# Kernel tuning notes

Measured on AMD Instinct MI355X. Metric: run time of the kernel, lower is better.

The kernel has to match this reference:

```python
import jax, jax.numpy as jnp
import numpy as np

H = 1024


def setup_inputs() -> dict:
    key = jax.random.key(0)
    ks = jax.random.split(key, 7)
    x = jax.random.normal(ks[0], (8, 2048, H), dtype=jnp.float32)
    s = 1.0 / np.sqrt(H)
    Wq = jax.random.normal(ks[1], (H, H), dtype=jnp.float32) * s
    bq = jnp.zeros((H,), dtype=jnp.float32)
    Wk = jax.random.normal(ks[2], (H, H), dtype=jnp.float32) * s
    bk = jnp.zeros((H,), dtype=jnp.float32)
    Wv = jax.random.normal(ks[3], (H, H), dtype=jnp.float32) * s
    bv = jnp.zeros((H,), dtype=jnp.float32)
    return {"x": x, "Wq": Wq, "bq": bq, "Wk": Wk, "bk": bk, "Wv": Wv, "bv": bv}


def reference(x, Wq, bq, Wk, bk, Wv, bv):
    # q,k,v: [B,S,H]
    q = jnp.einsum('bsh,hd->bsd', x, Wq) + bq
    k = jnp.einsum('bsh,hd->bsd', x, Wk) + bk
    v = jnp.einsum('bsh,hd->bsd', x, Wv) + bv
    scale = 1.0 / jnp.sqrt(jnp.asarray(x.shape[-1], dtype=x.dtype))
    scores = jnp.einsum('bqd,bkd->bqk', q, k) * scale  # [B,S,S]
    attn = jax.nn.softmax(scores, axis=-1)
    return jnp.einsum('bqk,bkd->bqd', attn, v)
```

## Files before the change

kernel.cpp:

```cpp
#include <hip/hip_runtime.h>

typedef _Float16 half8  __attribute__((ext_vector_type(8)));
typedef _Float16 half4v __attribute__((ext_vector_type(4)));
typedef float    floatx4 __attribute__((ext_vector_type(4)));

#define GLD_LDS16(g, l)                                                        \
  __builtin_amdgcn_global_load_lds(                                            \
      (const __attribute__((address_space(1))) void*)(g),                      \
      (__attribute__((address_space(3))) void*)(l), 16, 0, 0)

#define SBAR() __builtin_amdgcn_s_barrier()
#define WAITVM2() asm volatile("s_waitcnt vmcnt(2)" ::: "memory")
#define WAITVM0() asm volatile("s_waitcnt vmcnt(0)" ::: "memory")
#define SCHED0() __builtin_amdgcn_sched_barrier(0)


#define STG_A(c, ht, ko)                                                       \
  do {                                                                         \
    GLD_LDS16(A0 + (size_t)(ht) * lda128 + (ko),                               \
              &lds[(c) * 32768 + ((ht) * 1024 + wid * 128) * 8]);              \
    GLD_LDS16(A1 + (size_t)(ht) * lda128 + (ko),                               \
              &lds[(c) * 32768 + ((ht) * 1024 + wid * 128 + 64) * 8]);         \
  } while (0)
#define STG_B(c, ht, ko)                                                       \
  do {                                                                         \
    GLD_LDS16(B0 + (size_t)(ht) * ldb128 + (ko),                               \
              &lds[(c) * 32768 + 16384 + ((ht) * 1024 + wid * 128) * 8]);      \
    GLD_LDS16(B1 + (size_t)(ht) * ldb128 + (ko),                               \
              &lds[(c) * 32768 + 16384 + ((ht) * 1024 + wid * 128 + 64) * 8]); \
  } while (0)

#define RDA(dst, c, mt, ks)                                                    \
  do {                                                                         \
    const int ra_ = wm + (mt) * 16 + lr;                                       \
    dst = *(const half8*)&lds[(c) * 32768 +                                    \
                              (ra_ * 8 + (((ks) * 4 + lk) ^ (ra_ & 7))) * 8];  \
  } while (0)
#define RDB(dst, c, nt, ks)                                                    \
  do {                                                                         \
    const int rb_ = wn + (nt) * 16 + lr;                                       \
    dst = *(const half8*)&lds[(c) * 32768 + 16384 +                            \
                              (rb_ * 8 + (((ks) * 4 + lk) ^ (rb_ & 7))) * 8];  \
  } while (0)

#define MM4x2(MB, NB, BF)                                                      \
  do {                                                                         \
    _Pragma("unroll") for (int mt_ = 0; mt_ < 4; ++mt_)                        \
        _Pragma("unroll") for (int n_ = 0; n_ < 2; ++n_)                       \
            _Pragma("unroll") for (int ks_ = 0; ks_ < 2; ++ks_)                \
                acc[(MB) + mt_][(NB) + n_] =                                   \
        __builtin_amdgcn_mfma_f32_16x16x32_f16(                                \
            af[mt_][ks_], BF[n_][ks_], acc[(MB) + mt_][(NB) + n_], 0, 0, 0);   \
  } while (0)

#define KBLOCK(CUR, KT)                                                        \
  do {                                                                         \
    const int ko_ = ((KT) + 1) << 6;                                           \
    const bool pf_ = ((KT) + 1 < NT);                                          \
       \
    if (pf_) {                                                                 \
      STG_A(1 - (CUR), 0, ko_);                                                \
      WAITVM2();                                                               \
    } else {                                                                   \
      WAITVM0();                                                               \
    }                                                                          \
    SBAR();                                                                    \
    SCHED0();                                                                  \
    RDA(af[0][0], CUR, 0, 0); RDA(af[0][1], CUR, 0, 1);                        \
    RDA(af[1][0], CUR, 1, 0); RDA(af[1][1], CUR, 1, 1);                        \
    RDA(af[2][0], CUR, 2, 0); RDA(af[2][1], CUR, 2, 1);                        \
    RDA(af[3][0], CUR, 3, 0); RDA(af[3][1], CUR, 3, 1);                        \
    RDB(bf0[0][0], CUR, 0, 0); RDB(bf0[0][1], CUR, 0, 1);                      \
    RDB(bf0[1][0], CUR, 1, 0); RDB(bf0[1][1], CUR, 1, 1);                      \
    SBAR();                                                                    \
    SCHED0();                                                                  \
    __builtin_amdgcn_s_setprio(1);                                             \
    MM4x2(0, 0, bf0);                                                          \
    __builtin_amdgcn_s_setprio(0);                                             \
    SBAR();                                                                    \
                \
    RDB(bf1[0][0], CUR, 2, 0); RDB(bf1[0][1], CUR, 2, 1);                      \
    RDB(bf1[1][0], CUR, 3, 0); RDB(bf1[1][1], CUR, 3, 1);                      \
    if (pf_) STG_B(1 - (CUR), 0, ko_);                                         \
    SBAR();                                                                    \
    SCHED0();                                                                  \
    __builtin_amdgcn_s_setprio(1);                                             \
    MM4x2(0, 2, bf1);                                                          \
    __builtin_amdgcn_s_setprio(0);                                             \
    SBAR();                                                                    \
                        \
    RDA(af[0][0], CUR, 4, 0); RDA(af[0][1], CUR, 4, 1);                        \
    RDA(af[1][0], CUR, 5, 0); RDA(af[1][1], CUR, 5, 1);                        \
    RDA(af[2][0], CUR, 6, 0); RDA(af[2][1], CUR, 6, 1);                        \
    RDA(af[3][0], CUR, 7, 0); RDA(af[3][1], CUR, 7, 1);                        \
    if (pf_) STG_A(1 - (CUR), 1, ko_);                                         \
    SBAR();                                                                    \
    SCHED0();                                                                  \
    __builtin_amdgcn_s_setprio(1);                                             \
    MM4x2(4, 2, bf1);                                                          \
    __builtin_amdgcn_s_setprio(0);                                             \
    SBAR();                                                                    \
             \
    if (pf_) STG_B(1 - (CUR), 1, ko_);                                         \
    SBAR();                                                                    \
    SCHED0();                                                                  \
    __builtin_amdgcn_s_setprio(1);                                             \
    MM4x2(4, 0, bf0);                                                          \
    __builtin_amdgcn_s_setprio(0);                                             \
    SBAR();                                                                    \
  } while (0)

template <int EPI>
__global__ __launch_bounds__(512, 2) void gemm_bt(
    const _Float16* __restrict__ A, const _Float16* __restrict__ B,
    void* __restrict__ Cv, void* __restrict__ Cv2, int lda, int ldb, int ldc,
    int kdim, long long sAz, long long sBz, long long sCz,
    const float* __restrict__ b0, const float* __restrict__ b1,
    const float* __restrict__ b2, float* __restrict__ rowsum, float scale) {
  __shared__ _Float16 lds[65536];

  const int bid = blockIdx.x;
  int z, m0, n0;
  if (EPI == 0) {
    const int xcd = bid & 7, j = bid >> 3;
    z = j >> 5;
    m0 = (xcd * 8 + ((j >> 2) & 7)) * 256;
    n0 = (j & 3) * 256;
  } else if (EPI == 2) {
    z = bid & 7;
    const int j = bid >> 3;
    m0 = (j >> 3) * 256;
    n0 = (j & 7) * 256;
  } else {
    z = bid & 7;
    const int j = bid >> 3;
    m0 = (j >> 2) * 256;
    n0 = (j & 3) * 256;
  }

  A += (size_t)z * sAz;
  B += (size_t)z * sBz;

  const int tid = threadIdx.x;
  const int wid = tid >> 6;
  const int lane = tid & 63;
  const int wm = (wid & 1) * 128;
  const int wn = (wid >> 1) * 64;
  const int lr = lane & 15;
  const int lk = lane >> 4;

  floatx4 acc[8][4];
#pragma unroll
  for (int i = 0; i < 8; ++i)
#pragma unroll
    for (int j = 0; j < 4; ++j)
#pragma unroll
      for (int r = 0; r < 4; ++r) acc[i][j][r] = 0.f;

  const int s0 = wid * 128 + lane;
  const int s1 = s0 + 64;
  const int r0 = s0 >> 3, c0 = (s0 & 7) ^ (r0 & 7);
  const int r1 = s1 >> 3, c1 = (s1 & 7) ^ (r1 & 7);
  const _Float16* A0 = A + (size_t)(m0 + r0) * lda + c0 * 8;
  const _Float16* A1 = A + (size_t)(m0 + r1) * lda + c1 * 8;
  const _Float16* B0 = B + (size_t)(n0 + r0) * ldb + c0 * 8;
  const _Float16* B1 = B + (size_t)(n0 + r1) * ldb + c1 * 8;
  const size_t lda128 = (size_t)lda * 128;
  const size_t ldb128 = (size_t)ldb * 128;

  const int NT = kdim >> 6;

  STG_A(0, 0, 0);
  STG_B(0, 0, 0);
  STG_A(0, 1, 0);
  STG_B(0, 1, 0);
  WAITVM0();
  SBAR();

  half8 af[4][2], bf0[2][2], bf1[2][2];

  for (int kt = 0; kt < NT; kt += 2) {
    KBLOCK(0, kt);
    KBLOCK(1, kt + 1);
  }

  if (EPI == 0) {
    const float* bias = (z == 0) ? b0 : ((z == 1) ? b1 : b2);
#pragma unroll
    for (int mt = 0; mt < 8; ++mt) {
#pragma unroll
      for (int nt = 0; nt < 4; ++nt) {
#pragma unroll
        for (int r = 0; r < 4; ++r) {
          const int gm = m0 + wm + mt * 16 + lk * 4 + r;
          const int gn = n0 + wn + nt * 16 + lr;
          const float v = acc[mt][nt][r] + bias[gn];
          if (z < 2) {
            ((_Float16*)Cv)[(size_t)z * 16777216 + (size_t)gm * 1024 + gn] =
                (_Float16)v;
          } else {
            const int b = gm >> 11, sseq = gm & 2047;
            ((_Float16*)Cv2)[(size_t)b * 2097152 + (size_t)gn * 2048 + sseq] =
                (_Float16)v;
          }
        }
      }
    }
  } else if (EPI == 2) {
    const float c1 = scale * 1.44269504f;
    const float c0e = -5.77078016f;
    _Float16* Sout = (_Float16*)Cv + (size_t)z * sCz;
    float* rs = rowsum + z * 2048;
#pragma unroll
    for (int mt = 0; mt < 8; ++mt) {
#pragma unroll
      for (int r = 0; r < 4; ++r) {
        const int gm = m0 + wm + mt * 16 + lk * 4 + r;
        float part = 0.f;
#pragma unroll
        for (int nt = 0; nt < 4; ++nt) {
          const int gn = n0 + wn + nt * 16 + lr;
          const float p = exp2f(fmaf(acc[mt][nt][r], c1, c0e));
          const _Float16 ph = (_Float16)p;
          Sout[(size_t)gm * ldc + gn] = ph;
          part += (float)ph;
        }
#pragma unroll
        for (int o = 1; o < 16; o <<= 1) part += __shfl_xor(part, o);
        if (lr == 0) atomicAdd(&rs[gm], part);
      }
    }
  } else {
    float* O = (float*)Cv + (size_t)z * sCz;
    const float* rs = rowsum + z * 2048;
#pragma unroll
    for (int mt = 0; mt < 8; ++mt) {
#pragma unroll
      for (int r = 0; r < 4; ++r) {
        const int gm = m0 + wm + mt * 16 + lk * 4 + r;
        const float inv = 1.0f / rs[gm];
#pragma unroll
        for (int nt = 0; nt < 4; ++nt) {
          const int gn = n0 + wn + nt * 16 + lr;
          O[(size_t)gm * ldc + gn] = acc[mt][nt][r] * inv;
        }
      }
    }
  }
}

__global__ __launch_bounds__(256) void prep(
    const float* __restrict__ x, _Float16* __restrict__ xb,
    const float* __restrict__ W0, const float* __restrict__ W1,
    const float* __restrict__ W2, _Float16* __restrict__ Wt) {
  const int bid = blockIdx.x;
  const int tid = threadIdx.x;
  if (bid < 16384) {
    const int i = bid * 256 + tid;
    const float4 v = ((const float4*)x)[i];
    half4v h;
    h[0] = (_Float16)v.x;
    h[1] = (_Float16)v.y;
    h[2] = (_Float16)v.z;
    h[3] = (_Float16)v.w;
    ((half4v*)xb)[i] = h;
    return;
  }
  __shared__ float tile[32][33];
  const int q = bid - 16384;
  const int bz = q >> 10;
  const int t = q & 1023;
  const int d0 = (t & 31) * 32, h0 = (t >> 5) * 32;
  const float* W = bz == 0 ? W0 : (bz == 1 ? W1 : W2);
  _Float16* T = Wt + (size_t)bz * 1048576;
  const int tx = tid & 31, ty = tid >> 5;
#pragma unroll
  for (int i = 0; i < 4; ++i)
    tile[ty + i * 8][tx] = W[(size_t)(h0 + ty + i * 8) * 1024 + d0 + tx];
  __syncthreads();
#pragma unroll
  for (int i = 0; i < 4; ++i)
    T[(size_t)(d0 + ty + i * 8) * 1024 + h0 + tx] =
        (_Float16)tile[tx][ty + i * 8];
}

extern "C" void kernel_launch(void* const* d_in, const int* in_sizes, int n_in,
                              void* d_out, int out_size, void* d_ws,
                              size_t ws_size, hipStream_t stream) {
  const float* x = (const float*)d_in[0];
  const float* Wq = (const float*)d_in[1];
  const float* bq = (const float*)d_in[2];
  const float* Wk = (const float*)d_in[3];
  const float* bk = (const float*)d_in[4];
  const float* Wv = (const float*)d_in[5];
  const float* bv = (const float*)d_in[6];
  float* out = (float*)d_out;

  char* w = (char*)d_ws;
  _Float16* xb = (_Float16*)(w);
  _Float16* Wt = (_Float16*)(w + 33554432);
  _Float16* QK = (_Float16*)(w + 39845888);
  _Float16* Vt = (_Float16*)(w + 106954752);
  _Float16* S = (_Float16*)(w + 140509184);
  float* rowsum = (float*)(w);

  prep<<<19456, 256, 0, stream>>>(x, xb, Wq, Wk, Wv, Wt);
  gemm_bt<0><<<768, 512, 0, stream>>>(xb, Wt, QK, Vt, 1024, 1024, 1024, 1024,
                                      0LL, 1048576LL, 0LL, bq, bk, bv, nullptr,
                                      1.f);
  hipMemsetAsync(rowsum, 0, 8 * 2048 * sizeof(float), stream);
  gemm_bt<2><<<512, 512, 0, stream>>>(QK, QK + 16777216, S, nullptr, 1024,
                                      1024, 2048, 1024, 2097152LL, 2097152LL,
                                      4194304LL, nullptr, nullptr, nullptr,
                                      rowsum, 0.03125f);
  gemm_bt<3><<<256, 512, 0, stream>>>(S, Vt, out, nullptr, 2048, 2048, 1024,
                                      2048, 4194304LL, 2097152LL, 2097152LL,
                                      nullptr, nullptr, nullptr, rowsum, 1.f);

  (void)in_sizes;
  (void)n_in;
  (void)out_size;
  (void)ws_size;
}
```

Baseline: 411.7 us.

## Add smaller-tile QKV projection GEMM kernel with higher occupancy

Replaces the 256x256-tile projection GEMM with a dedicated 256x128-tile kernel that uses a 32-wide K step, 48 KB of double-buffered LDS and launch bounds allowing 4 blocks per CU. The grid grows from 768 to 1536 blocks. The aim is to fill the GPU better and cut tail effects during the QKV projection. The cost is more global traffic per FLOP, since each block reuses less data, and an extra barrier per shorter K step. The attention GEMMs are kept as before, only renamed.

```diff
diff --git a/kernel.cpp b/kernel.cpp
--- a/kernel.cpp
+++ b/kernel.cpp
@@ -11,18 +11,138 @@
 
 #define SBAR() __builtin_amdgcn_s_barrier()
 #define WAITVM2() asm volatile("s_waitcnt vmcnt(2)" ::: "memory")
+#define WAITVM3() asm volatile("s_waitcnt vmcnt(3)" ::: "memory")
 #define WAITVM0() asm volatile("s_waitcnt vmcnt(0)" ::: "memory")
 #define SCHED0() __builtin_amdgcn_sched_barrier(0)
 
 
-#define STG_A(c, ht, ko)                                                       \
+#define SSTG(c, ko)                                                            \
+  do {                                                                         \
+    GLD_LDS16(gA0 + (ko), &lds[(c) * 12288 + tid * 8]);                        \
+    GLD_LDS16(gA1 + (ko), &lds[(c) * 12288 + (512 + tid) * 8]);               \
+    GLD_LDS16(gB0 + (ko), &lds[(c) * 12288 + 8192 + tid * 8]);                \
+  } while (0)
+
+#define SRDA(dst, c, mt)                                                       \
+  do {                                                                         \
+    const int ra_ = wm + (mt) * 16 + lr;                                       \
+    dst = *(const half8*)&lds[(c) * 12288 +                                    \
+                              (ra_ * 4 + (lk ^ ((ra_ >> 1) & 3))) * 8];        \
+  } while (0)
+#define SRDB(dst, c, nt)                                                       \
+  do {                                                                         \
+    const int rb_ = wn + (nt) * 16 + lr;                                       \
+    dst = *(const half8*)&lds[(c) * 12288 + 8192 +                             \
+                              (rb_ * 4 + (lk ^ ((rb_ >> 1) & 3))) * 8];        \
+  } while (0)
+
+#define SKBLOCK(CUR, KT)                                                       \
+  do {                                                                         \
+    const int ko_ = ((KT) + 1) << 5;                                           \
+    const bool pf_ = ((KT) + 1 < NT);                                          \
+    if (pf_) {                                                                 \
+      SSTG(1 - (CUR), ko_);                                                    \
+      WAITVM3();                                                               \
+    } else {                                                                   \
+      WAITVM0();                                                               \
+    }                                                                          \
+    SBAR();                                                                    \
+    SCHED0();                                                                  \
+    half8 af[4], bf[4];                                                        \
+    SRDA(af[0], CUR, 0); SRDA(af[1], CUR, 1);                                  \
+    SRDA(af[2], CUR, 2); SRDA(af[3], CUR, 3);                                  \
+    SRDB(bf[0], CUR, 0); SRDB(bf[1], CUR, 1);                                  \
+    SRDB(bf[2], CUR, 2); SRDB(bf[3], CUR, 3);                                  \
+    __builtin_amdgcn_s_setprio(1);                                             \
+    _Pragma("unroll") for (int mt_ = 0; mt_ < 4; ++mt_)                        \
+        _Pragma("unroll") for (int nt_ = 0; nt_ < 4; ++nt_)                    \
+            acc[mt_][nt_] = __builtin_amdgcn_mfma_f32_16x16x32_f16(            \
+                af[mt_], bf[nt_], acc[mt_][nt_], 0, 0, 0);                     \
+    __builtin_amdgcn_s_setprio(0);                                             \
+    SBAR();                                                                    \
+  } while (0)
+
+__global__ __launch_bounds__(512, 4) void gemm_small(
+    const _Float16* __restrict__ A, const _Float16* __restrict__ B,
+    void* __restrict__ Cv, void* __restrict__ Cv2, int lda, int ldb,
+    int kdim, long long sBz, const float* __restrict__ b0,
+    const float* __restrict__ b1, const float* __restrict__ b2) {
+  __shared__ _Float16 lds[24576];
+
+  const int bid = blockIdx.x;
+  const int xcd = bid & 7, j = bid >> 3;
+  const int z = j >> 6;
+  const int m0 = (xcd * 8 + ((j >> 3) & 7)) * 256;
+  const int n0 = (j & 7) * 128;
+
+  B += (size_t)z * sBz;
+
+  const int tid = threadIdx.x;
+  const int wid = tid >> 6;
+  const int lane = tid & 63;
+  const int wm = (wid >> 1) * 64;
+  const int wn = (wid & 1) * 64;
+  const int lr = lane & 15;
+  const int lk = lane >> 4;
+
+  floatx4 acc[4][4];
+#pragma unroll
+  for (int i = 0; i < 4; ++i)
+#pragma unroll
+    for (int jj = 0; jj < 4; ++jj)
+#pragma unroll
+      for (int r = 0; r < 4; ++r) acc[i][jj][r] = 0.f;
+
+  const int sa0 = tid, sa1 = tid + 512, sb0 = tid;
+  const int ra0 = sa0 >> 2, ca0 = (sa0 & 3) ^ ((ra0 >> 1) & 3);
+  const int ra1 = sa1 >> 2, ca1 = (sa1 & 3) ^ ((ra1 >> 1) & 3);
+  const int rb0 = sb0 >> 2, cb0 = (sb0 & 3) ^ ((rb0 >> 1) & 3);
+  const _Float16* gA0 = A + (size_t)(m0 + ra0) * lda + ca0 * 8;
+  const _Float16* gA1 = A + (size_t)(m0 + ra1) * lda + ca1 * 8;
+  const _Float16* gB0 = B + (size_t)(n0 + rb0) * ldb + cb0 * 8;
+
+  const int NT = kdim >> 5;
+
+  SSTG(0, 0);
+  WAITVM0();
+  SBAR();
+
+  for (int kt = 0; kt < NT; kt += 2) {
+    SKBLOCK(0, kt);
+    SKBLOCK(1, kt + 1);
+  }
+
+  const float* bias = (z == 0) ? b0 : ((z == 1) ? b1 : b2);
+#pragma unroll
+  for (int mt = 0; mt < 4; ++mt) {
+#pragma unroll
+    for (int nt = 0; nt < 4; ++nt) {
+#pragma unroll
+      for (int r = 0; r < 4; ++r) {
+        const int gm = m0 + wm + mt * 16 + lk * 4 + r;
+        const int gn = n0 + wn + nt * 16 + lr;
+        const float v = acc[mt][nt][r] + bias[gn];
+        if (z < 2) {
+          ((_Float16*)Cv)[(size_t)z * 16777216 + (size_t)gm * 1024 + gn] =
+              (_Float16)v;
+        } else {
+          const int b = gm >> 11, sseq = gm & 2047;
+          ((_Float16*)Cv2)[(size_t)b * 2097152 + (size_t)gn * 2048 + sseq] =
+              (_Float16)v;
+        }
+      }
+    }
+  }
+}
+
+#define BSTG_A(c, ht, ko)                                                      \
   do {                                                                         \
     GLD_LDS16(A0 + (size_t)(ht) * lda128 + (ko),                               \
               &lds[(c) * 32768 + ((ht) * 1024 + wid * 128) * 8]);              \
     GLD_LDS16(A1 + (size_t)(ht) * lda128 + (ko),                               \
               &lds[(c) * 32768 + ((ht) * 1024 + wid * 128 + 64) * 8]);         \
   } while (0)
-#define STG_B(c, ht, ko)                                                       \
+#define BSTG_B(c, ht, ko)                                                      \
   do {                                                                         \
     GLD_LDS16(B0 + (size_t)(ht) * ldb128 + (ko),                               \
               &lds[(c) * 32768 + 16384 + ((ht) * 1024 + wid * 128) * 8]);      \
@@ -30,20 +150,20 @@
               &lds[(c) * 32768 + 16384 + ((ht) * 1024 + wid * 128 + 64) * 8]); \
   } while (0)
 
-#define RDA(dst, c, mt, ks)                                                    \
+#define BRDA(dst, c, mt, ks)                                                   \
   do {                                                                         \
     const int ra_ = wm + (mt) * 16 + lr;                                       \
     dst = *(const half8*)&lds[(c) * 32768 +                                    \
                               (ra_ * 8 + (((ks) * 4 + lk) ^ (ra_ & 7))) * 8];  \
   } while (0)
-#define RDB(dst, c, nt, ks)                                                    \
+#define BRDB(dst, c, nt, ks)                                                   \
   do {                                                                         \
     const int rb_ = wn + (nt) * 16 + lr;                                       \
     dst = *(const half8*)&lds[(c) * 32768 + 16384 +                            \
                               (rb_ * 8 + (((ks) * 4 + lk) ^ (rb_ & 7))) * 8];  \
   } while (0)
 
-#define MM4x2(MB, NB, BF)                                                      \
+#define BMM4x2(MB, NB, BF)                                                     \
   do {                                                                         \
     _Pragma("unroll") for (int mt_ = 0; mt_ < 4; ++mt_)                        \
         _Pragma("unroll") for (int n_ = 0; n_ < 2; ++n_)                       \
@@ -53,80 +173,70 @@
             af[mt_][ks_], BF[n_][ks_], acc[(MB) + mt_][(NB) + n_], 0, 0, 0);   \
   } while (0)
 
-#define KBLOCK(CUR, KT)                                                        \
+#define BKBLOCK(CUR, KT)                                                       \
   do {                                                                         \
     const int ko_ = ((KT) + 1) << 6;                                           \
     const bool pf_ = ((KT) + 1 < NT);                                          \
-       \
     if (pf_) {                                                                 \
-      STG_A(1 - (CUR), 0, ko_);                                                \
+      BSTG_A(1 - (CUR), 0, ko_);                                               \
       WAITVM2();                                                               \
     } else {                                                                   \
       WAITVM0();                                                               \
     }                                                                          \
     SBAR();                                                                    \
     SCHED0();                                                                  \
-    RDA(af[0][0], CUR, 0, 0); RDA(af[0][1], CUR, 0, 1);                        \
-    RDA(af[1][0], CUR, 1, 0); RDA(af[1][1], CUR, 1, 1);                        \
-    RDA(af[2][0], CUR, 2, 0); RDA(af[2][1], CUR, 2, 1);                        \
-    RDA(af[3][0], CUR, 3, 0); RDA(af[3][1], CUR, 3, 1);                        \
-    RDB(bf0[0][0], CUR, 0, 0); RDB(bf0[0][1], CUR, 0, 1);                      \
-    RDB(bf0[1][0], CUR, 1, 0); RDB(bf0[1][1], CUR, 1, 1);                      \
+    BRDA(af[0][0], CUR, 0, 0); BRDA(af[0][1], CUR, 0, 1);                      \
+    BRDA(af[1][0], CUR, 1, 0); BRDA(af[1][1], CUR, 1, 1);                      \
+    BRDA(af[2][0], CUR, 2, 0); BRDA(af[2][1], CUR, 2, 1);                      \
+    BRDA(af[3][0], CUR, 3, 0); BRDA(af[3][1], CUR, 3, 1);                      \
+    BRDB(bf0[0][0], CUR, 0, 0); BRDB(bf0[0][1], CUR, 0, 1);                    \
+    BRDB(bf0[1][0], CUR, 1, 0); BRDB(bf0[1][1], CUR, 1, 1);                    \
     SBAR();                                                                    \
     SCHED0();                                                                  \
     __builtin_amdgcn_s_setprio(1);                                             \
-    MM4x2(0, 0, bf0);                                                          \
+    BMM4x2(0, 0, bf0);                                                         \
     __builtin_amdgcn_s_setprio(0);                                             \
     SBAR();                                                                    \
-                \
-    RDB(bf1[0][0], CUR, 2, 0); RDB(bf1[0][1], CUR, 2, 1);                      \
-    RDB(bf1[1][0], CUR, 3, 0); RDB(bf1[1][1], CUR, 3, 1);                      \
-    if (pf_) STG_B(1 - (CUR), 0, ko_);                                         \
+    BRDB(bf1[0][0], CUR, 2, 0); BRDB(bf1[0][1], CUR, 2, 1);                    \
+    BRDB(bf1[1][0], CUR, 3, 0); BRDB(bf1[1][1], CUR, 3, 1);                    \
+    if (pf_) BSTG_B(1 - (CUR), 0, ko_);                                        \
     SBAR();                                                                    \
     SCHED0();                                                                  \
     __builtin_amdgcn_s_setprio(1);                                             \
-    MM4x2(0, 2, bf1);                                                          \
+    BMM4x2(0, 2, bf1);                                                         \
     __builtin_amdgcn_s_setprio(0);                                             \
     SBAR();                                                                    \
-                        \
-    RDA(af[0][0], CUR, 4, 0); RDA(af[0][1], CUR, 4, 1);                        \
-    RDA(af[1][0], CUR, 5, 0); RDA(af[1][1], CUR, 5, 1);                        \
-    RDA(af[2][0], CUR, 6, 0); RDA(af[2][1], CUR, 6, 1);                        \
-    RDA(af[3][0], CUR, 7, 0); RDA(af[3][1], CUR, 7, 1);                        \
-    if (pf_) STG_A(1 - (CUR), 1, ko_);                                         \
+    BRDA(af[0][0], CUR, 4, 0); BRDA(af[0][1], CUR, 4, 1);                      \
+    BRDA(af[1][0], CUR, 5, 0); BRDA(af[1][1], CUR, 5, 1);                      \
+    BRDA(af[2][0], CUR, 6, 0); BRDA(af[2][1], CUR, 6, 1);                      \
+    BRDA(af[3][0], CUR, 7, 0); BRDA(af[3][1], CUR, 7, 1);                      \
+    if (pf_) BSTG_A(1 - (CUR), 1, ko_);                                        \
     SBAR();                                                                    \
     SCHED0();                                                                  \
     __builtin_amdgcn_s_setprio(1);                                             \
-    MM4x2(4, 2, bf1);                                                          \
+    BMM4x2(4, 2, bf1);                                                         \
     __builtin_amdgcn_s_setprio(0);                                             \
     SBAR();                                                                    \
-             \
-    if (pf_) STG_B(1 - (CUR), 1, ko_);                                         \
+    if (pf_) BSTG_B(1 - (CUR), 1, ko_);                                        \
     SBAR();                                                                    \
     SCHED0();                                                                  \
     __builtin_amdgcn_s_setprio(1);                                             \
-    MM4x2(4, 0, bf0);                                                          \
+    BMM4x2(4, 0, bf0);                                                         \
     __builtin_amdgcn_s_setprio(0);                                             \
     SBAR();                                                                    \
   } while (0)
 
 template <int EPI>
-__global__ __launch_bounds__(512, 2) void gemm_bt(
+__global__ __launch_bounds__(512, 2) void gemm_big(
     const _Float16* __restrict__ A, const _Float16* __restrict__ B,
-    void* __restrict__ Cv, void* __restrict__ Cv2, int lda, int ldb, int ldc,
-    int kdim, long long sAz, long long sBz, long long sCz,
-    const float* __restrict__ b0, const float* __restrict__ b1,
-    const float* __restrict__ b2, float* __restrict__ rowsum, float scale) {
+    void* __restrict__ Cv, int lda, int ldb, int ldc, int kdim,
+    long long sAz, long long sBz, long long sCz,
+    float* __restrict__ rowsum, float scale) {
   __shared__ _Float16 lds[65536];
 
   const int bid = blockIdx.x;
   int z, m0, n0;
-  if (EPI == 0) {
-    const int xcd = bid & 7, j = bid >> 3;
-    z = j >> 5;
-    m0 = (xcd * 8 + ((j >> 2) & 7)) * 256;
-    n0 = (j & 3) * 256;
-  } else if (EPI == 2) {
+  if (EPI == 2) {
     z = bid & 7;
     const int j = bid >> 3;
     m0 = (j >> 3) * 256;
@@ -153,9 +263,9 @@
 #pragma unroll
   for (int i = 0; i < 8; ++i)
 #pragma unroll
-    for (int j = 0; j < 4; ++j)
-#pragma unroll
-      for (int r = 0; r < 4; ++r) acc[i][j][r] = 0.f;
+    for (int jj = 0; jj < 4; ++jj)
+#pragma unroll
+      for (int r = 0; r < 4; ++r) acc[i][jj][r] = 0.f;
 
   const int s0 = wid * 128 + lane;
   const int s1 = s0 + 64;
@@ -170,44 +280,22 @@
 
   const int NT = kdim >> 6;
 
-  STG_A(0, 0, 0);
-  STG_B(0, 0, 0);
-  STG_A(0, 1, 0);
-  STG_B(0, 1, 0);
+  BSTG_A(0, 0, 0);
+  BSTG_B(0, 0, 0);
+  BSTG_A(0, 1, 0);
+  BSTG_B(0, 1, 0);
   WAITVM0();
   SBAR();
 
   half8 af[4][2], bf0[2][2], bf1[2][2];
 
   for (int kt = 0; kt < NT; kt += 2) {
-    KBLOCK(0, kt);
-    KBLOCK(1, kt + 1);
-  }
-
-  if (EPI == 0) {
-    const float* bias = (z == 0) ? b0 : ((z == 1) ? b1 : b2);
-#pragma unroll
-    for (int mt = 0; mt < 8; ++mt) {
-#pragma unroll
-      for (int nt = 0; nt < 4; ++nt) {
-#pragma unroll
-        for (int r = 0; r < 4; ++r) {
-          const int gm = m0 + wm + mt * 16 + lk * 4 + r;
-          const int gn = n0 + wn + nt * 16 + lr;
-          const float v = acc[mt][nt][r] + bias[gn];
-          if (z < 2) {
-            ((_Float16*)Cv)[(size_t)z * 16777216 + (size_t)gm * 1024 + gn] =
-                (_Float16)v;
-          } else {
-            const int b = gm >> 11, sseq = gm & 2047;
-            ((_Float16*)Cv2)[(size_t)b * 2097152 + (size_t)gn * 2048 + sseq] =
-                (_Float16)v;
-          }
-        }
-      }
-    }
-  } else if (EPI == 2) {
-    const float c1 = scale * 1.44269504f;
+    BKBLOCK(0, kt);
+    BKBLOCK(1, kt + 1);
+  }
+
+  if (EPI == 2) {
+    const float c1f = scale * 1.44269504f;
     const float c0e = -5.77078016f;
     _Float16* Sout = (_Float16*)Cv + (size_t)z * sCz;
     float* rs = rowsum + z * 2048;
@@ -220,7 +308,7 @@
 #pragma unroll
         for (int nt = 0; nt < 4; ++nt) {
           const int gn = n0 + wn + nt * 16 + lr;
-          const float p = exp2f(fmaf(acc[mt][nt][r], c1, c0e));
+          const float p = exp2f(fmaf(acc[mt][nt][r], c1f, c0e));
           const _Float16 ph = (_Float16)p;
           Sout[(size_t)gm * ldc + gn] = ph;
           part += (float)ph;
@@ -305,17 +393,15 @@
   float* rowsum = (float*)(w);
 
   prep<<<19456, 256, 0, stream>>>(x, xb, Wq, Wk, Wv, Wt);
-  gemm_bt<0><<<768, 512, 0, stream>>>(xb, Wt, QK, Vt, 1024, 1024, 1024, 1024,
-                                      0LL, 1048576LL, 0LL, bq, bk, bv, nullptr,
-                                      1.f);
+  gemm_small<<<1536, 512, 0, stream>>>(xb, Wt, QK, Vt, 1024, 1024, 1024,
+                                       1048576LL, bq, bk, bv);
   hipMemsetAsync(rowsum, 0, 8 * 2048 * sizeof(float), stream);
-  gemm_bt<2><<<512, 512, 0, stream>>>(QK, QK + 16777216, S, nullptr, 1024,
-                                      1024, 2048, 1024, 2097152LL, 2097152LL,
-                                      4194304LL, nullptr, nullptr, nullptr,
-                                      rowsum, 0.03125f);
-  gemm_bt<3><<<256, 512, 0, stream>>>(S, Vt, out, nullptr, 2048, 2048, 1024,
-                                      2048, 4194304LL, 2097152LL, 2097152LL,
-                                      nullptr, nullptr, nullptr, rowsum, 1.f);
+  gemm_big<2><<<512, 512, 0, stream>>>(QK, QK + 16777216, S, 1024, 1024, 2048,
+                                       1024, 2097152LL, 2097152LL, 4194304LL,
+                                       rowsum, 0.03125f);
+  gemm_big<3><<<256, 512, 0, stream>>>(S, Vt, out, 2048, 2048, 1024, 2048,
+                                       4194304LL, 2097152LL, 2097152LL,
+                                       rowsum, 1.f);
 
   (void)in_sizes;
   (void)n_in;
```

Result: slower. 443.9 us (+7.8%).
